# Performance work log

Measured on AMD Instinct MI355X. Metric: run time of the kernel, lower is better.

The kernel has to match this reference:

```python
import jax, jax.numpy as jnp
import numpy as np
from jax import lax

C = 16
FIRE_RATE = 0.5
STEP_SIZE = 1.0


def _fixed_kernel():
    _i = np.array([0, 1, 0], dtype=np.float32)
    I = np.outer(_i, _i)
    dx = (np.outer([1, 2, 1], [-1, 0, 1]) / 8.0).astype(np.float32)
    dy = dx.T
    lap = np.array([[0.25, 0.5, 0.25], [0.5, -3, 0.5], [0.25, 0.5, 0.25]], dtype=np.float32)
    av = np.ones((3, 3), dtype=np.float32) / 9.0
    k = np.stack([I, dx, dy, lap, av], -1)            # [3,3,5]
    k = np.tile(k, (1, 1, C))                          # [3,3,5*C], channel-major blocks of 5
    return jnp.asarray(k[:, :, None, :])               # HWIO [3,3,1,5*C]

KERNEL = _fixed_kernel()


def setup_inputs() -> dict:
    key = jax.random.key(0)
    ks = jax.random.split(key, 5)
    B, S = 4, 512
    x = jax.random.normal(ks[0], (B, S, S, C), jnp.float32)
    noise = jax.random.normal(ks[1], (B, S, S, 1), jnp.float32)
    W1 = jax.random.normal(ks[2], (5 * C, 4 * C), jnp.float32) * (1.0 / np.sqrt(5 * C))
    b1 = jnp.zeros((4 * C,), jnp.float32)
    W2 = jax.random.normal(ks[3], (4 * C, 2 * C), jnp.float32) * (1.0 / np.sqrt(4 * C))
    b2 = jnp.zeros((2 * C,), jnp.float32)
    W3 = jax.random.normal(ks[4], (2 * C, C), jnp.float32) * (1.0 / np.sqrt(2 * C))
    b3 = jnp.zeros((C,), jnp.float32)
    return {"x": x, "noise": noise, "W1": W1, "b1": b1, "W2": W2, "b2": b2, "W3": W3, "b3": b3}


def _swish(z):
    return z * jax.nn.sigmoid(z)


def reference(x, noise, W1, b1, W2, b2, W3, b3):
    # perceive: depthwise 3x3 conv with 5 fixed kernels per channel -> [B,H,W,5*C]
    y = lax.conv_general_dilated(
        x, KERNEL, window_strides=(1, 1), padding="SAME",
        dimension_numbers=("NHWC", "HWIO", "NHWC"), feature_group_count=C)
    # 3-layer 1x1 conv MLP
    h = _swish(jnp.einsum("bhwc,cd->bhwd", y, W1) + b1)
    h = _swish(jnp.einsum("bhwc,cd->bhwd", h, W2) + b2)
    dx = (jnp.einsum("bhwc,cd->bhwd", h, W3) + b3) * STEP_SIZE
    # stochastic update mask: normal noise <= fire_rate
    update_mask = (noise <= FIRE_RATE).astype(jnp.float32)  # [B,H,W,1]
    return x + dx * update_mask
```

## Files before the change

kernel.cpp:

```cpp
#include <hip/hip_runtime.h>

typedef __bf16 bf16x8 __attribute__((ext_vector_type(8)));
typedef float f32x4 __attribute__((ext_vector_type(4)));

#define S 512
#define CH 16

__device__ __forceinline__ float swishf(float z) {
    float e = __expf(-z);
    return z * __builtin_amdgcn_rcpf(1.0f + e);
}

__global__ void prep_weights(const float* __restrict__ W1, const float* __restrict__ b1,
                             const float* __restrict__ W2, const float* __restrict__ b2,
                             const float* __restrict__ W3, const float* __restrict__ b3,
                             __bf16* __restrict__ wsf, float* __restrict__ wsb)
{
    int idx = blockIdx.x * 256 + threadIdx.x;
    if (idx < 17 * 512) {
        int frag = idx >> 9;
        int lane = (idx >> 3) & 63;
        int j = idx & 7;
        int lr = lane & 15, lg = lane >> 4;
        float v = 0.0f;
        if (frag < 12) {
            int u = frag / 3, tt = frag - u * 3;
            int k = tt * 32 + lg * 8 + j;
            if (k < 80) v = W1[k * 64 + u * 16 + lr];
        } else if (frag < 16) {
            int f2 = frag - 12;
            int u = f2 >> 1, tt = f2 & 1;
            int k = tt * 32 + lg * 8 + j;
            v = W2[k * 32 + u * 16 + lr];
        } else {
            int k = lg * 8 + j;
            v = W3[k * 16 + lr];
        }
        wsf[idx] = (__bf16)v;
    }
    if (blockIdx.x == 0) {
        int t = threadIdx.x;
        if (t < 64) wsb[t] = b1[t];
        else if (t < 96) wsb[t] = b2[t - 64];
        else if (t < 112) wsb[t] = b3[t - 96];
    }
}

__global__ __launch_bounds__(256) void nca_fused(
    const float* __restrict__ x, const float* __restrict__ noise,
    const __bf16* __restrict__ wsf, const float* __restrict__ wsb,
    float* __restrict__ out)
{
    __shared__ float xs[3 * 66 * 20];
    __shared__ unsigned int yb[64 * 52];
    __shared__ __bf16 h1s[64 * 72];
    __shared__ __bf16 h2s[64 * 40];

    const int tid = threadIdx.x;
    const int strip = blockIdx.x;
    const int w0 = (strip & 7) * 64;
    const int hrow = (strip >> 3) & (S - 1);
    const int bb = strip >> 12;

    const int lane = tid & 63;
    const int wv = tid >> 6;
    const int lr = lane & 15, lg = lane >> 4;

    const bf16x8* __restrict__ wfp = reinterpret_cast<const bf16x8*>(wsf);
    bf16x8 w1f[4][3], w2f[2][2], w3f;
#pragma unroll
    for (int u = 0; u < 4; ++u)
#pragma unroll
        for (int t = 0; t < 3; ++t) w1f[u][t] = wfp[(u * 3 + t) * 64 + lane];
#pragma unroll
    for (int u = 0; u < 2; ++u)
#pragma unroll
        for (int t = 0; t < 2; ++t) w2f[u][t] = wfp[(12 + u * 2 + t) * 64 + lane];
    w3f = wfp[16 * 64 + lane];
    float b1v[4], b2v[2], b3v;
#pragma unroll
    for (int u = 0; u < 4; ++u) b1v[u] = wsb[u * 16 + lr];
#pragma unroll
    for (int u = 0; u < 2; ++u) b2v[u] = wsb[64 + u * 16 + lr];
    b3v = wsb[96 + lr];

    for (int i = tid; i < 792; i += 256) {
        int r = i / 264;
        int q = i - r * 264;
        int w = w0 - 1 + (q >> 2);
        int c4 = (q & 3) << 2;
        int gr = hrow - 1 + r;
        float4 v = make_float4(0.f, 0.f, 0.f, 0.f);
        if ((unsigned)gr < (unsigned)S && (unsigned)w < (unsigned)S)
            v = *reinterpret_cast<const float4*>(x + ((bb * S + gr) * S + w) * CH + c4);
        *reinterpret_cast<float4*>(&xs[(r * 66 + (w - w0 + 1)) * 20 + c4]) = v;
    }
    __syncthreads();

    {
        const int p = lane;
        const int g = wv;
        float A[3][3][4];
#pragma unroll
        for (int r = 0; r < 3; ++r)
#pragma unroll
            for (int d = 0; d < 3; ++d) {
                float4 t4 = *reinterpret_cast<const float4*>(&xs[(r * 66 + p + d) * 20 + g * 4]);
                A[r][d][0] = t4.x; A[r][d][1] = t4.y; A[r][d][2] = t4.z; A[r][d][3] = t4.w;
            }
        unsigned short fs[20];
#pragma unroll
        for (int cc = 0; cc < 4; ++cc) {
            float cw0 = A[0][0][cc] + 2.f * A[1][0][cc] + A[2][0][cc];
            float cw1 = A[0][1][cc] + 2.f * A[1][1][cc] + A[2][1][cc];
            float cw2 = A[0][2][cc] + 2.f * A[1][2][cc] + A[2][2][cc];
            float rw0 = A[0][0][cc] + 2.f * A[0][1][cc] + A[0][2][cc];
            float rw2 = A[2][0][cc] + 2.f * A[2][1][cc] + A[2][2][cc];
            float ctr = A[1][1][cc];
            float fI  = ctr;
            float fdx = (cw2 - cw0) * 0.125f;
            float fdy = (rw2 - rw0) * 0.125f;
            float flp = 0.25f * (cw0 + 2.f * cw1 + cw2) - 4.f * ctr;
            float fav = ((cw0 + cw1 + cw2) - (A[1][0][cc] + A[1][1][cc] + A[1][2][cc])) * (1.f / 9.f);
            fs[cc * 5 + 0] = __builtin_bit_cast(unsigned short, (__bf16)fI);
            fs[cc * 5 + 1] = __builtin_bit_cast(unsigned short, (__bf16)fdx);
            fs[cc * 5 + 2] = __builtin_bit_cast(unsigned short, (__bf16)fdy);
            fs[cc * 5 + 3] = __builtin_bit_cast(unsigned short, (__bf16)flp);
            fs[cc * 5 + 4] = __builtin_bit_cast(unsigned short, (__bf16)fav);
        }
        unsigned int* dst = &yb[p * 52 + g * 10];
#pragma unroll
        for (int m = 0; m < 10; ++m)
            dst[m] = (unsigned int)fs[2 * m] | ((unsigned int)fs[2 * m + 1] << 16);
        if (g == 3) {
#pragma unroll
            for (int m = 0; m < 8; ++m) yb[p * 52 + 40 + m] = 0u;
        }
    }
    __syncthreads();

    const int mt = wv;
    bf16x8 a1[3];
#pragma unroll
    for (int t = 0; t < 3; ++t)
        a1[t] = *reinterpret_cast<const bf16x8*>(&yb[(mt * 16 + lr) * 52 + t * 16 + lg * 4]);
#pragma unroll
    for (int u = 0; u < 4; ++u) {
        f32x4 acc = {0.f, 0.f, 0.f, 0.f};
#pragma unroll
        for (int t = 0; t < 3; ++t)
            acc = __builtin_amdgcn_mfma_f32_16x16x32_bf16(a1[t], w1f[u][t], acc, 0, 0, 0);
#pragma unroll
        for (int r = 0; r < 4; ++r) {
            float h = swishf(acc[r] + b1v[u]);
            h1s[(mt * 16 + lg * 4 + r) * 72 + u * 16 + lr] = (__bf16)h;
        }
    }
    __syncthreads();

    bf16x8 a2[2];
#pragma unroll
    for (int t = 0; t < 2; ++t)
        a2[t] = *reinterpret_cast<const bf16x8*>(&h1s[(mt * 16 + lr) * 72 + t * 32 + lg * 8]);
#pragma unroll
    for (int u = 0; u < 2; ++u) {
        f32x4 acc = {0.f, 0.f, 0.f, 0.f};
#pragma unroll
        for (int t = 0; t < 2; ++t)
            acc = __builtin_amdgcn_mfma_f32_16x16x32_bf16(a2[t], w2f[u][t], acc, 0, 0, 0);
#pragma unroll
        for (int r = 0; r < 4; ++r) {
            float h = swishf(acc[r] + b2v[u]);
            h2s[(mt * 16 + lg * 4 + r) * 40 + u * 16 + lr] = (__bf16)h;
        }
    }
    __syncthreads();

    bf16x8 a3 = *reinterpret_cast<const bf16x8*>(&h2s[(mt * 16 + lr) * 40 + lg * 8]);
    f32x4 acc = {0.f, 0.f, 0.f, 0.f};
    acc = __builtin_amdgcn_mfma_f32_16x16x32_bf16(a3, w3f, acc, 0, 0, 0);
#pragma unroll
    for (int r = 0; r < 4; ++r) {
        int prow = mt * 16 + lg * 4 + r;
        int pix = (bb * S + hrow) * S + (w0 + prow);
        float cx = xs[(66 + prow + 1) * 20 + lr];
        float m = (noise[pix] <= 0.5f) ? 1.f : 0.f;
        out[pix * CH + lr] = cx + (acc[r] + b3v) * m;
    }
}

extern "C" void kernel_launch(void* const* d_in, const int* in_sizes, int n_in,
                              void* d_out, int out_size, void* d_ws, size_t ws_size,
                              hipStream_t stream)
{
    const float* x     = (const float*)d_in[0];
    const float* noise = (const float*)d_in[1];
    const float* W1    = (const float*)d_in[2];
    const float* b1    = (const float*)d_in[3];
    const float* W2    = (const float*)d_in[4];
    const float* b2    = (const float*)d_in[5];
    const float* W3    = (const float*)d_in[6];
    const float* b3    = (const float*)d_in[7];
    __bf16* wsf = (__bf16*)d_ws;
    float*  wsb = (float*)((char*)d_ws + 17408);
    float*  out = (float*)d_out;

    hipLaunchKernelGGL(prep_weights, dim3(34), dim3(256), 0, stream,
                       W1, b1, W2, b2, W3, b3, wsf, wsb);
    hipLaunchKernelGGL(nca_fused, dim3(4 * 512 * 8), dim3(256), 0, stream,
                       x, noise, wsf, wsb, out);
}
```

Before: 210.3 us.

## Restructure NCA kernel: per-wave rows, direct global stencil loads, 32x32 MFMA layer one

Each block now handles four rows (one per wave) of 64 pixels instead of one row, so the grid is four times smaller. Bf16 weights are staged once into LDS per block instead of being held in registers. The shared-memory x tile and perception buffer are gone: each lane loads its 3x3 neighbourhood straight from global memory and builds the first-layer A fragments in registers. The first layer uses 32x32x16 MFMA with the 80 inputs packed without padding. The goal is to remove LDS staging and block-wide barriers and to raise occupancy, at the cost of redundant global and cache loads for the stencil halo.

```diff
diff --git a/kernel.cpp b/kernel.cpp
--- a/kernel.cpp
+++ b/kernel.cpp
@@ -2,41 +2,49 @@
 
 typedef __bf16 bf16x8 __attribute__((ext_vector_type(8)));
 typedef float f32x4 __attribute__((ext_vector_type(4)));
+typedef float f32x16 __attribute__((ext_vector_type(16)));
+typedef short short8 __attribute__((ext_vector_type(8)));
 
 #define S 512
 #define CH 16
 
+#define ELT(v, c) ((c)==0 ? (v).x : (c)==1 ? (v).y : (c)==2 ? (v).z : (v).w)
+
 __device__ __forceinline__ float swishf(float z) {
-    float e = __expf(-z);
-    return z * __builtin_amdgcn_rcpf(1.0f + e);
+    return z * __builtin_amdgcn_rcpf(1.0f + __expf(-z));
 }
 
 __global__ void prep_weights(const float* __restrict__ W1, const float* __restrict__ b1,
                              const float* __restrict__ W2, const float* __restrict__ b2,
                              const float* __restrict__ W3, const float* __restrict__ b3,
-                             __bf16* __restrict__ wsf, float* __restrict__ wsb)
+                             short* __restrict__ wsf, float* __restrict__ wsb)
 {
     int idx = blockIdx.x * 256 + threadIdx.x;
-    if (idx < 17 * 512) {
-        int frag = idx >> 9;
-        int lane = (idx >> 3) & 63;
-        int j = idx & 7;
-        int lr = lane & 15, lg = lane >> 4;
-        float v = 0.0f;
-        if (frag < 12) {
-            int u = frag / 3, tt = frag - u * 3;
-            int k = tt * 32 + lg * 8 + j;
-            if (k < 80) v = W1[k * 64 + u * 16 + lr];
-        } else if (frag < 16) {
-            int f2 = frag - 12;
-            int u = f2 >> 1, tt = f2 & 1;
-            int k = tt * 32 + lg * 8 + j;
-            v = W2[k * 32 + u * 16 + lr];
+    if (idx < 7680) {
+        float v;
+        if (idx < 5120) {
+            int fi = idx >> 9, rem = idx & 511;
+            int lane = rem >> 3, j = rem & 7;
+            int n = fi / 5, s = fi - n * 5;
+            int blk = lane >> 5, colw = lane & 31;
+            int m = s * 8 + j, cc = m / 5, f = m - cc * 5;
+            int row = (blk * 8 + cc) * 5 + f;
+            v = W1[row * 64 + n * 32 + colw];
+        } else if (idx < 7168) {
+            int i2 = idx - 5120;
+            int fi = i2 >> 9, rem = i2 & 511;
+            int lane = rem >> 3, j = rem & 7;
+            int u2 = fi >> 1, t = fi & 1;
+            int k = t * 32 + (lane >> 4) * 8 + j;
+            v = W2[k * 32 + u2 * 16 + (lane & 15)];
         } else {
-            int k = lg * 8 + j;
-            v = W3[k * 16 + lr];
-        }
-        wsf[idx] = (__bf16)v;
+            int i3 = idx - 7168;
+            int lane = i3 >> 3, j = i3 & 7;
+            int k = (lane >> 4) * 8 + j;
+            v = W3[k * 16 + (lane & 15)];
+        }
+        __bf16 b = (__bf16)v;
+        wsf[idx] = __builtin_bit_cast(short, b);
     }
     if (blockIdx.x == 0) {
         int t = threadIdx.x;
@@ -46,146 +54,149 @@
     }
 }
 
-__global__ __launch_bounds__(256) void nca_fused(
+__global__ __launch_bounds__(256, 4) void nca_fused(
     const float* __restrict__ x, const float* __restrict__ noise,
-    const __bf16* __restrict__ wsf, const float* __restrict__ wsb,
+    const short* __restrict__ wsf, const float* __restrict__ wsb,
     float* __restrict__ out)
 {
-    __shared__ float xs[3 * 66 * 20];
-    __shared__ unsigned int yb[64 * 52];
-    __shared__ __bf16 h1s[64 * 72];
-    __shared__ __bf16 h2s[64 * 40];
+    __shared__ short wlds[7680];
+    __shared__ __bf16 h1s[4][32][72];
+    __shared__ __bf16 h2s[4][16][40];
 
     const int tid = threadIdx.x;
-    const int strip = blockIdx.x;
-    const int w0 = (strip & 7) * 64;
-    const int hrow = (strip >> 3) & (S - 1);
-    const int bb = strip >> 12;
-
+    {
+        const int4* src = reinterpret_cast<const int4*>(wsf);
+        int4* dst = reinterpret_cast<int4*>(wlds);
+        for (int i = tid; i < 960; i += 256) dst[i] = src[i];
+    }
+    __syncthreads();
+
+    const int bid = blockIdx.x;
+    const int st = bid & 7;
+    const int rg = (bid >> 3) & 127;
+    const int bb = bid >> 10;
+    const int wv = tid >> 6;
     const int lane = tid & 63;
-    const int wv = tid >> 6;
+    const int col = lane & 31, hi = lane >> 5;
     const int lr = lane & 15, lg = lane >> 4;
-
-    const bf16x8* __restrict__ wfp = reinterpret_cast<const bf16x8*>(wsf);
-    bf16x8 w1f[4][3], w2f[2][2], w3f;
-#pragma unroll
-    for (int u = 0; u < 4; ++u)
-#pragma unroll
-        for (int t = 0; t < 3; ++t) w1f[u][t] = wfp[(u * 3 + t) * 64 + lane];
-#pragma unroll
-    for (int u = 0; u < 2; ++u)
-#pragma unroll
-        for (int t = 0; t < 2; ++t) w2f[u][t] = wfp[(12 + u * 2 + t) * 64 + lane];
-    w3f = wfp[16 * 64 + lane];
-    float b1v[4], b2v[2], b3v;
-#pragma unroll
-    for (int u = 0; u < 4; ++u) b1v[u] = wsb[u * 16 + lr];
-#pragma unroll
-    for (int u = 0; u < 2; ++u) b2v[u] = wsb[64 + u * 16 + lr];
+    const int row = rg * 4 + wv;
+
+    float b1v[2], b2v[2], b3v;
+    b1v[0] = wsb[col];        b1v[1] = wsb[32 + col];
+    b2v[0] = wsb[64 + lr];    b2v[1] = wsb[80 + lr];
     b3v = wsb[96 + lr];
 
-    for (int i = tid; i < 792; i += 256) {
-        int r = i / 264;
-        int q = i - r * 264;
-        int w = w0 - 1 + (q >> 2);
-        int c4 = (q & 3) << 2;
-        int gr = hrow - 1 + r;
-        float4 v = make_float4(0.f, 0.f, 0.f, 0.f);
-        if ((unsigned)gr < (unsigned)S && (unsigned)w < (unsigned)S)
-            v = *reinterpret_cast<const float4*>(x + ((bb * S + gr) * S + w) * CH + c4);
-        *reinterpret_cast<float4*>(&xs[(r * 66 + (w - w0 + 1)) * 20 + c4]) = v;
-    }
-    __syncthreads();
-
-    {
-        const int p = lane;
-        const int g = wv;
-        float A[3][3][4];
-#pragma unroll
-        for (int r = 0; r < 3; ++r)
-#pragma unroll
-            for (int d = 0; d < 3; ++d) {
-                float4 t4 = *reinterpret_cast<const float4*>(&xs[(r * 66 + p + d) * 20 + g * 4]);
-                A[r][d][0] = t4.x; A[r][d][1] = t4.y; A[r][d][2] = t4.z; A[r][d][3] = t4.w;
-            }
-        unsigned short fs[20];
-#pragma unroll
-        for (int cc = 0; cc < 4; ++cc) {
-            float cw0 = A[0][0][cc] + 2.f * A[1][0][cc] + A[2][0][cc];
-            float cw1 = A[0][1][cc] + 2.f * A[1][1][cc] + A[2][1][cc];
-            float cw2 = A[0][2][cc] + 2.f * A[1][2][cc] + A[2][2][cc];
-            float rw0 = A[0][0][cc] + 2.f * A[0][1][cc] + A[0][2][cc];
-            float rw2 = A[2][0][cc] + 2.f * A[2][1][cc] + A[2][2][cc];
-            float ctr = A[1][1][cc];
-            float fI  = ctr;
-            float fdx = (cw2 - cw0) * 0.125f;
-            float fdy = (rw2 - rw0) * 0.125f;
-            float flp = 0.25f * (cw0 + 2.f * cw1 + cw2) - 4.f * ctr;
-            float fav = ((cw0 + cw1 + cw2) - (A[1][0][cc] + A[1][1][cc] + A[1][2][cc])) * (1.f / 9.f);
-            fs[cc * 5 + 0] = __builtin_bit_cast(unsigned short, (__bf16)fI);
-            fs[cc * 5 + 1] = __builtin_bit_cast(unsigned short, (__bf16)fdx);
-            fs[cc * 5 + 2] = __builtin_bit_cast(unsigned short, (__bf16)fdy);
-            fs[cc * 5 + 3] = __builtin_bit_cast(unsigned short, (__bf16)flp);
-            fs[cc * 5 + 4] = __builtin_bit_cast(unsigned short, (__bf16)fav);
-        }
-        unsigned int* dst = &yb[p * 52 + g * 10];
-#pragma unroll
-        for (int m = 0; m < 10; ++m)
-            dst[m] = (unsigned int)fs[2 * m] | ((unsigned int)fs[2 * m + 1] << 16);
-        if (g == 3) {
-#pragma unroll
-            for (int m = 0; m < 8; ++m) yb[p * 52 + 40 + m] = 0u;
-        }
-    }
-    __syncthreads();
-
-    const int mt = wv;
-    bf16x8 a1[3];
-#pragma unroll
-    for (int t = 0; t < 3; ++t)
-        a1[t] = *reinterpret_cast<const bf16x8*>(&yb[(mt * 16 + lr) * 52 + t * 16 + lg * 4]);
-#pragma unroll
-    for (int u = 0; u < 4; ++u) {
-        f32x4 acc = {0.f, 0.f, 0.f, 0.f};
-#pragma unroll
-        for (int t = 0; t < 3; ++t)
-            acc = __builtin_amdgcn_mfma_f32_16x16x32_bf16(a1[t], w1f[u][t], acc, 0, 0, 0);
-#pragma unroll
-        for (int r = 0; r < 4; ++r) {
-            float h = swishf(acc[r] + b1v[u]);
-            h1s[(mt * 16 + lg * 4 + r) * 72 + u * 16 + lr] = (__bf16)h;
-        }
-    }
-    __syncthreads();
-
-    bf16x8 a2[2];
-#pragma unroll
-    for (int t = 0; t < 2; ++t)
-        a2[t] = *reinterpret_cast<const bf16x8*>(&h1s[(mt * 16 + lr) * 72 + t * 32 + lg * 8]);
-#pragma unroll
-    for (int u = 0; u < 2; ++u) {
-        f32x4 acc = {0.f, 0.f, 0.f, 0.f};
-#pragma unroll
-        for (int t = 0; t < 2; ++t)
-            acc = __builtin_amdgcn_mfma_f32_16x16x32_bf16(a2[t], w2f[u][t], acc, 0, 0, 0);
-#pragma unroll
-        for (int r = 0; r < 4; ++r) {
-            float h = swishf(acc[r] + b2v[u]);
-            h2s[(mt * 16 + lg * 4 + r) * 40 + u * 16 + lr] = (__bf16)h;
-        }
-    }
-    __syncthreads();
-
-    bf16x8 a3 = *reinterpret_cast<const bf16x8*>(&h2s[(mt * 16 + lr) * 40 + lg * 8]);
-    f32x4 acc = {0.f, 0.f, 0.f, 0.f};
-    acc = __builtin_amdgcn_mfma_f32_16x16x32_bf16(a3, w3f, acc, 0, 0, 0);
-#pragma unroll
-    for (int r = 0; r < 4; ++r) {
-        int prow = mt * 16 + lg * 4 + r;
-        int pix = (bb * S + hrow) * S + (w0 + prow);
-        float cx = xs[(66 + prow + 1) * 20 + lr];
-        float m = (noise[pix] <= 0.5f) ? 1.f : 0.f;
-        out[pix * CH + lr] = cx + (acc[r] + b3v) * m;
+    const bool rv0 = row > 0, rv2 = row < S - 1;
+    const float* xb = x + (size_t)bb * S * S * CH;
+    const short8* wf = reinterpret_cast<const short8*>(wlds);
+
+#pragma unroll
+    for (int mt = 0; mt < 2; ++mt) {
+        const int px0 = st * 64 + mt * 32;
+        const bool colInt = (px0 != 0) && (px0 != 480);
+        const int p = col;
+
+        short8 af[5];
+#pragma unroll
+        for (int qi = 0; qi < 2; ++qi) {
+            const int q = hi * 2 + qi;
+            float4 A[3][3];
+#pragma unroll
+            for (int rr = 0; rr < 3; ++rr) {
+                bool rok = (rr == 0) ? rv0 : (rr == 2 ? rv2 : true);
+                if (rok) {
+                    const float* rp = xb + (size_t)(row - 1 + rr) * S * CH + q * 4;
+                    if (colInt) {
+                        const float* bp = rp + (px0 + p - 1) * CH;
+                        A[rr][0] = *reinterpret_cast<const float4*>(bp);
+                        A[rr][1] = *reinterpret_cast<const float4*>(bp + CH);
+                        A[rr][2] = *reinterpret_cast<const float4*>(bp + 2 * CH);
+                    } else {
+#pragma unroll
+                        for (int d = 0; d < 3; ++d) {
+                            int c = px0 + p - 1 + d;
+                            int cl = min(max(c, 0), S - 1);
+                            float4 v = *reinterpret_cast<const float4*>(rp + cl * CH);
+                            if ((unsigned)c >= (unsigned)S) v = make_float4(0.f, 0.f, 0.f, 0.f);
+                            A[rr][d] = v;
+                        }
+                    }
+                } else {
+                    A[rr][0] = make_float4(0.f, 0.f, 0.f, 0.f);
+                    A[rr][1] = A[rr][0]; A[rr][2] = A[rr][0];
+                }
+            }
+#pragma unroll
+            for (int cc = 0; cc < 4; ++cc) {
+                float a00 = ELT(A[0][0], cc), a01 = ELT(A[0][1], cc), a02 = ELT(A[0][2], cc);
+                float a10 = ELT(A[1][0], cc), a11 = ELT(A[1][1], cc), a12 = ELT(A[1][2], cc);
+                float a20 = ELT(A[2][0], cc), a21 = ELT(A[2][1], cc), a22 = ELT(A[2][2], cc);
+                float cw0 = a00 + 2.f * a10 + a20;
+                float cw1 = a01 + 2.f * a11 + a21;
+                float cw2 = a02 + 2.f * a12 + a22;
+                float rw0 = a00 + 2.f * a01 + a02;
+                float rw2 = a20 + 2.f * a21 + a22;
+                float fI  = a11;
+                float fdx = (cw2 - cw0) * 0.125f;
+                float fdy = (rw2 - rw0) * 0.125f;
+                float flp = 0.25f * (cw0 + 2.f * cw1 + cw2) - 4.f * a11;
+                float fav = ((cw0 + cw1 + cw2) - (a10 + a11 + a12)) * (1.f / 9.f);
+                const int mb = (qi * 4 + cc) * 5;
+                af[(mb + 0) >> 3][(mb + 0) & 7] = __builtin_bit_cast(short, (__bf16)fI);
+                af[(mb + 1) >> 3][(mb + 1) & 7] = __builtin_bit_cast(short, (__bf16)fdx);
+                af[(mb + 2) >> 3][(mb + 2) & 7] = __builtin_bit_cast(short, (__bf16)fdy);
+                af[(mb + 3) >> 3][(mb + 3) & 7] = __builtin_bit_cast(short, (__bf16)flp);
+                af[(mb + 4) >> 3][(mb + 4) & 7] = __builtin_bit_cast(short, (__bf16)fav);
+            }
+        }
+
+#pragma unroll
+        for (int n = 0; n < 2; ++n) {
+            f32x16 acc = {};
+#pragma unroll
+            for (int s = 0; s < 5; ++s) {
+                bf16x8 a = __builtin_bit_cast(bf16x8, af[s]);
+                bf16x8 b = __builtin_bit_cast(bf16x8, wf[(n * 5 + s) * 64 + lane]);
+                acc = __builtin_amdgcn_mfma_f32_32x32x16_bf16(a, b, acc, 0, 0, 0);
+            }
+#pragma unroll
+            for (int r = 0; r < 16; ++r) {
+                int p2 = (r & 3) + 8 * (r >> 2) + 4 * hi;
+                h1s[wv][p2][n * 32 + col] = (__bf16)swishf(acc[r] + b1v[n]);
+            }
+        }
+
+#pragma unroll
+        for (int sub = 0; sub < 2; ++sub) {
+            bf16x8 a2[2];
+#pragma unroll
+            for (int t = 0; t < 2; ++t)
+                a2[t] = *reinterpret_cast<const bf16x8*>(&h1s[wv][sub * 16 + lr][t * 32 + lg * 8]);
+#pragma unroll
+            for (int u2 = 0; u2 < 2; ++u2) {
+                f32x4 acc2 = {};
+#pragma unroll
+                for (int t = 0; t < 2; ++t) {
+                    bf16x8 b = __builtin_bit_cast(bf16x8, wf[640 + (u2 * 2 + t) * 64 + lane]);
+                    acc2 = __builtin_amdgcn_mfma_f32_16x16x32_bf16(a2[t], b, acc2, 0, 0, 0);
+                }
+#pragma unroll
+                for (int r = 0; r < 4; ++r)
+                    h2s[wv][lg * 4 + r][u2 * 16 + lr] = (__bf16)swishf(acc2[r] + b2v[u2]);
+            }
+            bf16x8 a3 = *reinterpret_cast<const bf16x8*>(&h2s[wv][lr][lg * 8]);
+            bf16x8 b3f = __builtin_bit_cast(bf16x8, wf[896 + lane]);
+            f32x4 acc3 = {};
+            acc3 = __builtin_amdgcn_mfma_f32_16x16x32_bf16(a3, b3f, acc3, 0, 0, 0);
+#pragma unroll
+            for (int r = 0; r < 4; ++r) {
+                int pxg = px0 + sub * 16 + lg * 4 + r;
+                size_t pix = (size_t)(bb * S + row) * S + pxg;
+                float cx = x[pix * CH + lr];
+                float msk = (noise[pix] <= 0.5f) ? 1.f : 0.f;
+                out[pix * CH + lr] = cx + (acc3[r] + b3v) * msk;
+            }
+        }
     }
 }
 
@@ -201,12 +212,12 @@
     const float* b2    = (const float*)d_in[5];
     const float* W3    = (const float*)d_in[6];
     const float* b3    = (const float*)d_in[7];
-    __bf16* wsf = (__bf16*)d_ws;
-    float*  wsb = (float*)((char*)d_ws + 17408);
-    float*  out = (float*)d_out;
-
-    hipLaunchKernelGGL(prep_weights, dim3(34), dim3(256), 0, stream,
+    short* wsf = (short*)d_ws;
+    float* wsb = (float*)((char*)d_ws + 15360);
+    float* out = (float*)d_out;
+
+    hipLaunchKernelGGL(prep_weights, dim3(30), dim3(256), 0, stream,
                        W1, b1, W2, b2, W3, b3, wsf, wsb);
-    hipLaunchKernelGGL(nca_fused, dim3(4 * 512 * 8), dim3(256), 0, stream,
+    hipLaunchKernelGGL(nca_fused, dim3(4 * 128 * 8), dim3(256), 0, stream,
                        x, noise, wsf, wsb, out);
 }
```

Measured after the change: 178.1 us. -15.3%, faster.
